# Kernel optimization log

Hardware: AMD Instinct MI355X
Metric: run time of the kernel (lower is better)

## Reference

```python
import jax, jax.numpy as jnp
import numpy as np

TEMP = 0.07  # module hardcodes self.temp = 0.07 regardless of ctor arg
N, C = 8192, 256


def setup_inputs() -> dict:
    key = jax.random.key(0)
    kq, kk = jax.random.split(key)
    q = jax.random.normal(kq, (N, C), dtype=jnp.float32)
    k = jax.random.normal(kk, (N, C), dtype=jnp.float32)
    return {"q": q, "k": k}


def reference(q, k):
    # Original builds logits = [l_pos, l_neg_row] per sample i where
    # l_pos = q_i . k_i and l_neg_row = q_i . k_j for j != i, then applies
    # CrossEntropyLoss with label 0. That logits row is exactly a permutation
    # of the full similarity row sim[i, :] = q_i @ k.T (diagonal = positive),
    # so CE(logits/T, 0) == logsumexp(sim_i/T) - sim_ii/T. Single fused GEMM
    # + row-wise logsumexp, identical math and gradients.
    sim = jnp.matmul(q, k.T) / TEMP            # [N, N]
    pos = jnp.diagonal(sim)                    # [N]
    lse = jax.nn.logsumexp(sim, axis=1)        # [N]
    return jnp.mean(lse - pos)                 # scalar loss
```

## Files before the change

### kernel.cpp

```cpp
#include <hip/hip_runtime.h>
#include <stdint.h>


#define N_ROWS 8192
#define C_DIM  256
#define BM     128
#define BN     64
#define SPLIT  8
#define JCOLS  (N_ROWS / SPLIT)
#define JTILES (JCOLS / BN)
#define TILE_B (BN * C_DIM * 2)

typedef __attribute__((ext_vector_type(8))) _Float16 half8;
typedef __attribute__((ext_vector_type(4))) _Float16 half4;
typedef __attribute__((ext_vector_type(4))) float    f32x4;

#if __has_builtin(__builtin_amdgcn_exp2f)
#define EXP2(x) __builtin_amdgcn_exp2f(x)
#else
#define EXP2(x) exp2f(x)
#endif
#if __has_builtin(__builtin_amdgcn_logf)
#define LOG2(x) __builtin_amdgcn_logf(x)
#else
#define LOG2(x) log2f(x)
#endif

__device__ __forceinline__ void gload_lds16(const void* g, void* l) {
  __builtin_amdgcn_global_load_lds(
      (const __attribute__((address_space(1))) unsigned int*)g,
      (__attribute__((address_space(3))) unsigned int*)l, 16, 0, 0);
}

__global__ void cvt_kernel(const float* __restrict__ q, const float* __restrict__ k,
                           _Float16* __restrict__ qh, _Float16* __restrict__ kh) {
  const float QS = 20.60992915555663f;
  int i = blockIdx.x * 256 + threadIdx.x;
  float4 qv = ((const float4*)q)[i];
  float4 kv = ((const float4*)k)[i];
  half4 qo, ko;
  qo[0] = (_Float16)(qv.x * QS); qo[1] = (_Float16)(qv.y * QS);
  qo[2] = (_Float16)(qv.z * QS); qo[3] = (_Float16)(qv.w * QS);
  ko[0] = (_Float16)kv.x; ko[1] = (_Float16)kv.y;
  ko[2] = (_Float16)kv.z; ko[3] = (_Float16)kv.w;
  ((half4*)qh)[i] = qo;
  ((half4*)kh)[i] = ko;
}

__launch_bounds__(256, 2)
__global__ void sim_lse_kernel(const _Float16* __restrict__ qh,
                               const _Float16* __restrict__ kh,
                               float* __restrict__ pM,
                               float* __restrict__ pS,
                               float* __restrict__ pP) {
  __shared__ __align__(16) _Float16 kt[2 * BN * C_DIM];
  const int tid  = threadIdx.x;
  const int lane = tid & 63;
  const int wave = tid >> 6;
  const int l15  = lane & 15;
  const int lg   = lane >> 4;

  const int rb   = blockIdx.x;
  const int sp   = blockIdx.y;
  const int row0 = rb * BM + wave * 32;

  half8 afrag[2][8];
#pragma unroll
  for (int g = 0; g < 2; ++g) {
    const _Float16* qr = qh + (size_t)(row0 + g * 16 + l15) * C_DIM + lg * 8;
#pragma unroll
    for (int f = 0; f < 8; ++f)
      afrag[g][f] = *(const half8*)(qr + f * 32);
  }

  float M[2][4], S[2][4], P[2][4];
#pragma unroll
  for (int g = 0; g < 2; ++g)
#pragma unroll
    for (int r = 0; r < 4; ++r) {
      M[g][r] = -__builtin_inff(); S[g][r] = 0.f; P[g][r] = -__builtin_inff();
    }

  int bbase[4];
#pragma unroll
  for (int cf = 0; cf < 4; ++cf) {
    int nl = cf * 16 + l15;
    bbase[cf] = nl * 512 + (((nl & 31) * 16) ^ (lg * 16));
  }

  const char* ksrc = (const char*)(kh + (size_t)sp * JCOLS * C_DIM);
  char* lds = (char*)kt;

#define STAGE(BUF, JT)                                                   \
  do {                                                                   \
    const char* src = ksrc + (size_t)(JT) * TILE_B;                      \
    char* dst = lds + (BUF) * TILE_B;                                    \
    _Pragma("unroll")                                                    \
    for (int it = 0; it < 8; ++it) {                                     \
      int linear = it * 4096 + tid * 16;                                 \
      int row = linear >> 9;                                             \
      int c16 = (linear >> 4) & 31;                                      \
      int gc  = c16 ^ (row & 31);                                        \
      gload_lds16(src + row * 512 + gc * 16, dst + linear);              \
    }                                                                    \
  } while (0)

  STAGE(0, 0);

  for (int jt = 0; jt < JTILES; ++jt) {
    const int cur = jt & 1;
    __syncthreads();
    if (jt + 1 < JTILES) STAGE(cur ^ 1, jt + 1);

    f32x4 acc[2][4];
#pragma unroll
    for (int g = 0; g < 2; ++g)
#pragma unroll
      for (int cf = 0; cf < 4; ++cf) { f32x4 z = {0.f, 0.f, 0.f, 0.f}; acc[g][cf] = z; }

    const char* buf = lds + cur * TILE_B;
#pragma unroll
    for (int ks = 0; ks < 8; ++ks) {
#pragma unroll
      for (int cf = 0; cf < 4; ++cf) {
        half8 b = *(const half8*)(buf + (bbase[cf] ^ (ks * 64)));
        acc[0][cf] = __builtin_amdgcn_mfma_f32_16x16x32_f16(afrag[0][ks], b, acc[0][cf], 0, 0, 0);
        acc[1][cf] = __builtin_amdgcn_mfma_f32_16x16x32_f16(afrag[1][ks], b, acc[1][cf], 0, 0, 0);
      }
    }

    const int j0 = sp * JCOLS + jt * BN;

#pragma unroll
    for (int g = 0; g < 2; ++g) {
      const int rg0 = row0 + g * 16;
      if (rg0 >= j0 && rg0 < j0 + BN) {
#pragma unroll
        for (int r = 0; r < 4; ++r) {
          int d = rg0 - j0 + lg * 4 + r;
#pragma unroll
          for (int cf = 0; cf < 4; ++cf)
            if (cf * 16 + l15 == d) P[g][r] = acc[g][cf][r];
        }
      }

#pragma unroll
      for (int r = 0; r < 4; ++r) {
        float v0 = acc[g][0][r], v1 = acc[g][1][r], v2 = acc[g][2][r], v3 = acc[g][3][r];
        float tmax = fmaxf(fmaxf(v0, v1), fmaxf(v2, v3));
        float newM  = fmaxf(M[g][r], tmax);
        float alpha = EXP2(M[g][r] - newM);
        float p = EXP2(v0 - newM) + EXP2(v1 - newM) +
                  EXP2(v2 - newM) + EXP2(v3 - newM);
        S[g][r] = fmaf(S[g][r], alpha, p);
        M[g][r] = newM;
      }
    }
  }

#pragma unroll
  for (int g = 0; g < 2; ++g)
#pragma unroll
    for (int r = 0; r < 4; ++r) {
#pragma unroll
      for (int off = 1; off < 16; off <<= 1) {
        float Mo = __shfl_xor(M[g][r], off);
        float So = __shfl_xor(S[g][r], off);
        float nm = fmaxf(M[g][r], Mo);
        S[g][r] = S[g][r] * EXP2(M[g][r] - nm) + So * EXP2(Mo - nm);
        M[g][r] = nm;
        P[g][r] = fmaxf(P[g][r], __shfl_xor(P[g][r], off));
      }
    }

  if (l15 == 0) {
#pragma unroll
    for (int g = 0; g < 2; ++g)
#pragma unroll
      for (int r = 0; r < 4; ++r) {
        int grow = row0 + g * 16 + lg * 4 + r;
        pM[(size_t)sp * N_ROWS + grow] = M[g][r];
        pS[(size_t)sp * N_ROWS + grow] = S[g][r];
        pP[(size_t)sp * N_ROWS + grow] = P[g][r];
      }
  }
}

__global__ void finish_kernel(const float* __restrict__ pM, const float* __restrict__ pS,
                              const float* __restrict__ pP, float* __restrict__ out) {
  const int tid = threadIdx.x;
  float accl = 0.f;
#pragma unroll
  for (int i = 0; i < N_ROWS / 1024; ++i) {
    int r = i * 1024 + tid;
    float m = -__builtin_inff();
#pragma unroll
    for (int s = 0; s < SPLIT; ++s) m = fmaxf(m, pM[s * N_ROWS + r]);
    float ssum = 0.f;
    float pos  = -__builtin_inff();
#pragma unroll
    for (int s = 0; s < SPLIT; ++s) {
      ssum = fmaf(pS[s * N_ROWS + r], EXP2(pM[s * N_ROWS + r] - m), ssum);
      pos = fmaxf(pos, pP[s * N_ROWS + r]);
    }
    accl += (m + LOG2(ssum)) - pos;
  }
#pragma unroll
  for (int off = 1; off < 64; off <<= 1) accl += __shfl_xor(accl, off);
  __shared__ float wsum[16];
  if ((tid & 63) == 0) wsum[tid >> 6] = accl;
  __syncthreads();
  if (tid < 64) {
    float v = (tid < 16) ? wsum[tid] : 0.f;
#pragma unroll
    for (int off = 1; off < 16; off <<= 1) v += __shfl_xor(v, off);
    if (tid == 0)
      out[0] = v * (0.69314718055994531f / (float)N_ROWS);
  }
}

extern "C" void kernel_launch(void* const* d_in, const int* in_sizes, int n_in,
                              void* d_out, int out_size, void* d_ws, size_t ws_size,
                              hipStream_t stream) {
  const float* q = (const float*)d_in[0];
  const float* k = (const float*)d_in[1];
  float* out = (float*)d_out;
  char* ws = (char*)d_ws;

  _Float16* qh = (_Float16*)ws;
  _Float16* kh = (_Float16*)(ws + (size_t)N_ROWS * C_DIM * 2);
  float* pM = (float*)(ws + (size_t)N_ROWS * C_DIM * 4);
  float* pS = pM + SPLIT * N_ROWS;
  float* pP = pS + SPLIT * N_ROWS;

  cvt_kernel<<<dim3(N_ROWS * C_DIM / 4 / 256), dim3(256), 0, stream>>>(q, k, qh, kh);
  sim_lse_kernel<<<dim3(N_ROWS / BM, SPLIT), dim3(256), 0, stream>>>(qh, kh, pM, pS, pP);
  finish_kernel<<<dim3(1), dim3(1024), 0, stream>>>(pM, pS, pP, out);
}
```

Before: 113.1 us.

## Software-pipeline softmax epilogue with next tile MFMAs and skip negligible exp chunks

Double-buffers the accumulator registers so the online logsumexp update for the previous tile is interleaved with the MFMA loop of the current tile, overlapping exp/max ALU work with matrix math. It also adds a wave-uniform skip of the exp/rescale update when every value in a chunk is more than 24 (log2 units) below the running max. The skip drops contributions smaller than about 2^-24 relative to the max, which slightly changes the numerics. Holding two accumulator sets raises register pressure under the 2-waves-per-SIMD launch bound.

```diff
diff --git a/kernel.cpp b/kernel.cpp
--- a/kernel.cpp
+++ b/kernel.cpp
@@ -10,6 +10,7 @@
 #define JCOLS  (N_ROWS / SPLIT)
 #define JTILES (JCOLS / BN)
 #define TILE_B (BN * C_DIM * 2)
+#define SKIP_D 24.0f
 
 typedef __attribute__((ext_vector_type(8))) _Float16 half8;
 typedef __attribute__((ext_vector_type(4))) _Float16 half4;
@@ -105,58 +106,99 @@
     }                                                                    \
   } while (0)
 
+#define DIAG(JT, ACC)                                                    \
+  do {                                                                   \
+    const int j0p = sp * JCOLS + (JT) * BN;                              \
+    _Pragma("unroll")                                                    \
+    for (int g = 0; g < 2; ++g) {                                        \
+      const int rg0 = row0 + g * 16;                                     \
+      if (rg0 >= j0p && rg0 < j0p + BN) {                                \
+        _Pragma("unroll")                                                \
+        for (int r = 0; r < 4; ++r) {                                    \
+          int d = rg0 - j0p + lg * 4 + r;                                \
+          _Pragma("unroll")                                              \
+          for (int cf = 0; cf < 4; ++cf)                                 \
+            if (cf * 16 + l15 == d) P[g][r] = (ACC)[g][cf][r];           \
+        }                                                                \
+      }                                                                  \
+    }                                                                    \
+  } while (0)
+
+#define CHUNK(ACC, G, R)                                                 \
+  do {                                                                   \
+    float v0 = (ACC)[G][0][R], v1 = (ACC)[G][1][R],                      \
+          v2 = (ACC)[G][2][R], v3 = (ACC)[G][3][R];                      \
+    float tmax = fmaxf(fmaxf(v0, v1), fmaxf(v2, v3));                    \
+    if (__any(tmax > M[G][R] - SKIP_D)) {                                \
+      float newM  = fmaxf(M[G][R], tmax);                                \
+      float alpha = EXP2(M[G][R] - newM);                                \
+      float p = EXP2(v0 - newM) + EXP2(v1 - newM) +                      \
+                EXP2(v2 - newM) + EXP2(v3 - newM);                       \
+      S[G][R] = fmaf(S[G][R], alpha, p);                                 \
+      M[G][R] = newM;                                                    \
+    }                                                                    \
+  } while (0)
+
+#define TILE_ITER(JT, ACCN, ACCP, DO_STAGE)                              \
+  do {                                                                   \
+    __syncthreads();                                                     \
+    if (DO_STAGE) STAGE(((JT) + 1) & 1, (JT) + 1);                       \
+    DIAG((JT) - 1, ACCP);                                                \
+    const char* buf = lds + ((JT) & 1) * TILE_B;                         \
+    _Pragma("unroll")                                                    \
+    for (int g = 0; g < 2; ++g)                                          \
+      _Pragma("unroll")                                                  \
+      for (int cf = 0; cf < 4; ++cf) {                                   \
+        f32x4 z = {0.f, 0.f, 0.f, 0.f}; (ACCN)[g][cf] = z;               \
+      }                                                                  \
+    _Pragma("unroll")                                                    \
+    for (int ks = 0; ks < 8; ++ks) {                                     \
+      _Pragma("unroll")                                                  \
+      for (int cf = 0; cf < 4; ++cf) {                                   \
+        half8 b = *(const half8*)(buf + (bbase[cf] ^ (ks * 64)));        \
+        (ACCN)[0][cf] = __builtin_amdgcn_mfma_f32_16x16x32_f16(          \
+            afrag[0][ks], b, (ACCN)[0][cf], 0, 0, 0);                    \
+        (ACCN)[1][cf] = __builtin_amdgcn_mfma_f32_16x16x32_f16(          \
+            afrag[1][ks], b, (ACCN)[1][cf], 0, 0, 0);                    \
+      }                                                                  \
+      CHUNK(ACCP, ks >> 2, ks & 3);                                      \
+    }                                                                    \
+  } while (0)
+
+  f32x4 accA[2][4], accB[2][4];
+
   STAGE(0, 0);
-
-  for (int jt = 0; jt < JTILES; ++jt) {
-    const int cur = jt & 1;
-    __syncthreads();
-    if (jt + 1 < JTILES) STAGE(cur ^ 1, jt + 1);
-
-    f32x4 acc[2][4];
+  __syncthreads();
+  STAGE(1, 1);
+
+  {
+    const char* buf = lds;
 #pragma unroll
     for (int g = 0; g < 2; ++g)
 #pragma unroll
-      for (int cf = 0; cf < 4; ++cf) { f32x4 z = {0.f, 0.f, 0.f, 0.f}; acc[g][cf] = z; }
-
-    const char* buf = lds + cur * TILE_B;
-#pragma unroll
-    for (int ks = 0; ks < 8; ++ks) {
+      for (int cf = 0; cf < 4; ++cf) { f32x4 z = {0.f, 0.f, 0.f, 0.f}; accA[g][cf] = z; }
+#pragma unroll
+    for (int ks = 0; ks < 8; ++ks)
 #pragma unroll
       for (int cf = 0; cf < 4; ++cf) {
         half8 b = *(const half8*)(buf + (bbase[cf] ^ (ks * 64)));
-        acc[0][cf] = __builtin_amdgcn_mfma_f32_16x16x32_f16(afrag[0][ks], b, acc[0][cf], 0, 0, 0);
-        acc[1][cf] = __builtin_amdgcn_mfma_f32_16x16x32_f16(afrag[1][ks], b, acc[1][cf], 0, 0, 0);
+        accA[0][cf] = __builtin_amdgcn_mfma_f32_16x16x32_f16(afrag[0][ks], b, accA[0][cf], 0, 0, 0);
+        accA[1][cf] = __builtin_amdgcn_mfma_f32_16x16x32_f16(afrag[1][ks], b, accA[1][cf], 0, 0, 0);
       }
-    }
-
-    const int j0 = sp * JCOLS + jt * BN;
-
-#pragma unroll
-    for (int g = 0; g < 2; ++g) {
-      const int rg0 = row0 + g * 16;
-      if (rg0 >= j0 && rg0 < j0 + BN) {
-#pragma unroll
-        for (int r = 0; r < 4; ++r) {
-          int d = rg0 - j0 + lg * 4 + r;
-#pragma unroll
-          for (int cf = 0; cf < 4; ++cf)
-            if (cf * 16 + l15 == d) P[g][r] = acc[g][cf][r];
-        }
-      }
-
-#pragma unroll
-      for (int r = 0; r < 4; ++r) {
-        float v0 = acc[g][0][r], v1 = acc[g][1][r], v2 = acc[g][2][r], v3 = acc[g][3][r];
-        float tmax = fmaxf(fmaxf(v0, v1), fmaxf(v2, v3));
-        float newM  = fmaxf(M[g][r], tmax);
-        float alpha = EXP2(M[g][r] - newM);
-        float p = EXP2(v0 - newM) + EXP2(v1 - newM) +
-                  EXP2(v2 - newM) + EXP2(v3 - newM);
-        S[g][r] = fmaf(S[g][r], alpha, p);
-        M[g][r] = newM;
-      }
-    }
-  }
+  }
+
+  for (int jt = 1; jt + 1 < JTILES; jt += 2) {
+    TILE_ITER(jt,     accB, accA, true);
+    TILE_ITER(jt + 1, accA, accB, true);
+  }
+  TILE_ITER(JTILES - 1, accB, accA, false);
+
+  DIAG(JTILES - 1, accB);
+#pragma unroll
+  for (int g = 0; g < 2; ++g)
+#pragma unroll
+    for (int r = 0; r < 4; ++r)
+      CHUNK(accB, g, r);
 
 #pragma unroll
   for (int g = 0; g < 2; ++g)
```

Measured after the change: 115.9 us. +2.5%, slower.
